# Performance work log

Hardware: AMD Instinct MI355X
Metric: run time of the kernel (lower is better)

Reference implementation:

```python
import jax, jax.numpy as jnp
import numpy as np

HID = 1024
HEADS = 16
HEAD_DIM = HID // HEADS
FFN = 4096
EPS = 1e-5


def setup_inputs() -> dict:
    key = jax.random.key(0)
    ks = jax.random.split(key, 12)
    s = lambda k, shape, fan_in: jax.random.normal(k, shape, jnp.float32) * (fan_in ** -0.5)
    return {
        "hidden_states": jax.random.normal(ks[0], (2, 2048, HID), jnp.float32),
        "Wq": s(ks[1], (HID, HID), HID),
        "Wk": s(ks[2], (HID, HID), HID),
        "Wv": s(ks[3], (HID, HID), HID),
        "Wo": s(ks[4], (HID, HID), HID),
        "W1": s(ks[5], (HID, FFN), HID),
        "b1": jnp.zeros((FFN,), jnp.float32),
        "W2": s(ks[6], (FFN, HID), FFN),
        "b2": jnp.zeros((HID,), jnp.float32),
        "ln1_scale": jnp.ones((HID,), jnp.float32),
        "ln1_shift": jnp.zeros((HID,), jnp.float32),
        "ln2_scale": jnp.ones((HID,), jnp.float32),
        "ln2_shift": jnp.zeros((HID,), jnp.float32),
    }


def _layer_norm(x, scale, shift):
    mean = jnp.mean(x, axis=-1, keepdims=True)
    var = jnp.var(x, axis=-1, keepdims=True)  # biased, matches unbiased=False
    return (x - mean) * jax.lax.rsqrt(var + EPS) * scale + shift


def _forward(hidden_states, Wq, Wk, Wv, Wo, W1, b1, W2, b2,
             ln1_scale, ln1_shift, ln2_scale, ln2_shift):
    bsz, seq_len, _ = hidden_states.shape
    residual = hidden_states
    x = _layer_norm(hidden_states, ln1_scale, ln1_shift)

    # q/k/v projections -> [b, h, s, d]
    def proj(W):
        return (x @ W).reshape(bsz, seq_len, HEADS, HEAD_DIM).transpose(0, 2, 1, 3)
    q, k, v = proj(Wq), proj(Wk), proj(Wv)

    scores = jnp.einsum("bhqd,bhkd->bhqk", q, k)
    causal = jnp.triu(jnp.ones((seq_len, seq_len), bool), k=1)
    scores = jnp.where(causal, -jnp.inf, scores) / (HEAD_DIM ** 0.5)
    attn = jax.nn.softmax(scores, axis=-1)  # dropout is identity in eval
    out = jnp.einsum("bhqk,bhkd->bhqd", attn, v)
    out = out.transpose(0, 2, 1, 3).reshape(bsz, seq_len, HID)
    hidden_states = residual + out @ Wo

    residual = hidden_states
    y = _layer_norm(hidden_states, ln2_scale, ln2_shift)
    y = jax.nn.gelu(y @ W1 + b1, approximate=False) @ W2 + b2  # torch nn.GELU default = exact erf
    return residual + y


def reference(hidden_states, Wq, Wk, Wv, Wo, W1, b1, W2, b2,
              ln1_scale, ln1_shift, ln2_scale, ln2_shift):
    return _forward(hidden_states, Wq, Wk, Wv, Wo, W1, b1, W2, b2,
                    ln1_scale, ln1_shift, ln2_scale, ln2_shift)
```

## Files before the change

### kernel.cpp

```cpp
#include <hip/hip_runtime.h>
#include <math.h>

using bf16x8 = __attribute__((ext_vector_type(8))) short;
using f32x4  = __attribute__((ext_vector_type(4))) float;

struct __align__(8) us4 { unsigned short x, y, z, w; };

__device__ __forceinline__ unsigned short f2b(float f) {
  union { float f; unsigned u; } v; v.f = f;
  unsigned r = v.u + 0x7FFFu + ((v.u >> 16) & 1u);
  return (unsigned short)(r >> 16);
}

#define GLDS(g, l) __builtin_amdgcn_global_load_lds(                        \
    (const __attribute__((address_space(1))) void*)(g),                    \
    (__attribute__((address_space(3))) void*)(l), 16, 0, 0)

__global__ void __launch_bounds__(256) transpose_w(
    const float* __restrict__ src, unsigned short* __restrict__ dst,
    int K, int N) {
  __shared__ float tile[32][33];
  const int n0 = blockIdx.x * 32, k0 = blockIdx.y * 32;
  const int tx = threadIdx.x & 31, ty = threadIdx.x >> 5;
#pragma unroll
  for (int i = 0; i < 32; i += 8)
    tile[ty + i][tx] = src[(size_t)(k0 + ty + i) * N + n0 + tx];
  __syncthreads();
#pragma unroll
  for (int i = 0; i < 32; i += 8)
    dst[(size_t)(n0 + ty + i) * K + k0 + tx] = f2b(tile[tx][ty + i]);
}

__global__ void __launch_bounds__(256) ln_kernel(
    const float* __restrict__ in, const float* __restrict__ scale,
    const float* __restrict__ shift, unsigned short* __restrict__ out) {
  const int row = blockIdx.x, t = threadIdx.x;
  const float4 v = ((const float4*)(in + (size_t)row * 1024))[t];
  float s  = v.x + v.y + v.z + v.w;
  float s2 = v.x * v.x + v.y * v.y + v.z * v.z + v.w * v.w;
#pragma unroll
  for (int off = 32; off; off >>= 1) {
    s  += __shfl_xor(s,  off);
    s2 += __shfl_xor(s2, off);
  }
  __shared__ float red[8];
  const int w = t >> 6, lane = t & 63;
  if (!lane) { red[w] = s; red[4 + w] = s2; }
  __syncthreads();
  s  = red[0] + red[1] + red[2] + red[3];
  s2 = red[4] + red[5] + red[6] + red[7];
  const float mean = s * (1.0f / 1024.0f);
  const float var  = s2 * (1.0f / 1024.0f) - mean * mean;
  const float rstd = rsqrtf(var + 1e-5f);
  const float4 sc = ((const float4*)scale)[t];
  const float4 sh = ((const float4*)shift)[t];
  us4 o;
  o.x = f2b((v.x - mean) * rstd * sc.x + sh.x);
  o.y = f2b((v.y - mean) * rstd * sc.y + sh.y);
  o.z = f2b((v.z - mean) * rstd * sc.z + sh.z);
  o.w = f2b((v.w - mean) * rstd * sc.w + sh.w);
  ((us4*)(out + (size_t)row * 1024))[t] = o;
}

template <int MODE, int BM>
__global__ void __launch_bounds__(256) gemm_bt(
    const unsigned short* __restrict__ A, const unsigned short* __restrict__ B,
    int K, int N,
    float* __restrict__ outf, unsigned short* __restrict__ outb,
    const float* __restrict__ bias, const float* __restrict__ resid,
    unsigned short* __restrict__ vt) {
  constexpr int WN = (BM == 128) ? 2 : 4;
  constexpr int NJ = 128 / (16 * WN);
  __shared__ unsigned short lA[BM * 64];
  __shared__ unsigned short lB[128 * 64];
  const int t = threadIdx.x, lane = t & 63;
  const int w = t >> 6, wm = w / WN, wn = w % WN;
  const int r16 = lane & 15, g = lane >> 4;
  const int m0 = blockIdx.x * BM, n0 = blockIdx.y * 128;

  f32x4 acc[4][NJ] = {};
  const int nkt = K >> 6;
  for (int kt = 0; kt < nkt; ++kt) {
    __syncthreads();
#pragma unroll
    for (int p = 0; p < BM / 32; ++p) {
      const int ci = t + p * 256;
      const int m = ci >> 3, cs = ci & 7;
      const int kb = cs ^ (m & 7);
      GLDS(A + (size_t)(m0 + m) * K + kt * 64 + kb * 8, &lA[ci * 8]);
    }
#pragma unroll
    for (int p = 0; p < 4; ++p) {
      const int ci = t + p * 256;
      const int m = ci >> 3, cs = ci & 7;
      const int kb = cs ^ (m & 7);
      GLDS(B + (size_t)(n0 + m) * K + kt * 64 + kb * 8, &lB[ci * 8]);
    }
    __syncthreads();
#pragma unroll
    for (int ks = 0; ks < 2; ++ks) {
      bf16x8 af[4], bfr[NJ];
#pragma unroll
      for (int i = 0; i < 4; ++i) {
        const int m = wm * 64 + i * 16 + r16;
        const int kb = ks * 4 + g;
        af[i] = *(const bf16x8*)&lA[((m << 3) + (kb ^ (m & 7))) << 3];
      }
#pragma unroll
      for (int j = 0; j < NJ; ++j) {
        const int n = wn * (16 * NJ) + j * 16 + r16;
        const int kb = ks * 4 + g;
        bfr[j] = *(const bf16x8*)&lB[((n << 3) + (kb ^ (n & 7))) << 3];
      }
#pragma unroll
      for (int i = 0; i < 4; ++i)
#pragma unroll
        for (int j = 0; j < NJ; ++j)
          acc[i][j] = __builtin_amdgcn_mfma_f32_16x16x32_bf16(
              af[i], bfr[j], acc[i][j], 0, 0, 0);
    }
  }

#pragma unroll
  for (int i = 0; i < 4; ++i) {
    const int row0 = m0 + wm * 64 + i * 16 + g * 4;
#pragma unroll
    for (int j = 0; j < NJ; ++j) {
      const int colb = n0 + wn * (16 * NJ) + j * 16;
      const int col = colb + r16;
      if constexpr (MODE == 0) {
        if (colb < 2048) {
#pragma unroll
          for (int r = 0; r < 4; ++r)
            outb[(size_t)(row0 + r) * 2048 + col] = f2b(acc[i][j][r]);
        } else {
          const int b = row0 >> 11, s0 = row0 & 2047;
          us4 pk;
          pk.x = f2b(acc[i][j][0]); pk.y = f2b(acc[i][j][1]);
          pk.z = f2b(acc[i][j][2]); pk.w = f2b(acc[i][j][3]);
          *(us4*)&vt[((size_t)b * 1024 + (col - 2048)) * 2048 + s0] = pk;
        }
      } else if constexpr (MODE == 1) {
#pragma unroll
        for (int r = 0; r < 4; ++r) {
          const size_t idx = (size_t)(row0 + r) * N + col;
          outf[idx] = acc[i][j][r] + resid[idx];
        }
      } else if constexpr (MODE == 2) {
#pragma unroll
        for (int r = 0; r < 4; ++r) {
          const float x = acc[i][j][r] + bias[col];
          const float ge = 0.5f * x * (1.0f + erff(x * 0.70710678118654752f));
          outb[(size_t)(row0 + r) * N + col] = f2b(ge);
        }
      } else {
#pragma unroll
        for (int r = 0; r < 4; ++r) {
          const size_t idx = (size_t)(row0 + r) * N + col;
          outf[idx] = acc[i][j][r] + bias[col] + resid[idx];
        }
      }
    }
  }
}

__global__ void __launch_bounds__(256) attn_kernel(
    const unsigned short* __restrict__ qk, const unsigned short* __restrict__ vt,
    unsigned short* __restrict__ obuf) {
  const int j = blockIdx.x, h = blockIdx.y, bb = blockIdx.z;
  const int t = threadIdx.x, lane = t & 63, w = t >> 6;
  const int r16 = lane & 15, g = lane >> 4;
  __shared__ unsigned short lK[2][64 * 64];
  __shared__ unsigned short lV[2][64 * 64];
  __shared__ unsigned short lP[4][16 * 72];

  const int qtA = j, qtB = 31 - j;
  const int ktmax = qtB;
  const int qrowA = qtA * 64 + w * 16 + r16;
  const int qrowB = qtB * 64 + w * 16 + r16;
  const float CE = 0.18033688011112042f;

  bf16x8 qfA[2], qfB[2];
  {
    const unsigned short* qa =
        qk + (size_t)(bb * 2048 + qrowA) * 2048 + h * 64;
    qfA[0] = *(const bf16x8*)(qa + g * 8);
    qfA[1] = *(const bf16x8*)(qa + 32 + g * 8);
    const unsigned short* qb =
        qk + (size_t)(bb * 2048 + qrowB) * 2048 + h * 64;
    qfB[0] = *(const bf16x8*)(qb + g * 8);
    qfB[1] = *(const bf16x8*)(qb + 32 + g * 8);
  }

  f32x4 accA[4] = {}, accB[4] = {};
  float mA = -3.0e38f, lA_ = 0.0f, mB = -3.0e38f, lB_ = 0.0f;

  auto stage = [&](int buf, int kt) {
    const int k0 = kt * 64;
#pragma unroll
    for (int p = 0; p < 2; ++p) {
      const int ci = t + p * 256;
      const int r = ci >> 3, cs = ci & 7;
      const int cb = cs ^ (r & 7);
      GLDS(qk + (size_t)(bb * 2048 + k0 + r) * 2048 + 1024 + h * 64 + cb * 8,
           &lK[buf][ci * 8]);
      GLDS(vt + ((size_t)bb * 1024 + h * 64 + r) * 2048 + k0 + cb * 8,
           &lV[buf][ci * 8]);
    }
  };

  auto flash_step = [&](const bf16x8* qf, f32x4* accO, float& mrun,
                        float& lrun, int qrow, bool diag, int k0, int cur) {
    f32x4 s[4] = {};
#pragma unroll
    for (int ks = 0; ks < 2; ++ks)
#pragma unroll
      for (int mt = 0; mt < 4; ++mt) {
        const int r = mt * 16 + r16, db = ks * 4 + g;
        const bf16x8 kf =
            *(const bf16x8*)&lK[cur][((r << 3) + (db ^ (r & 7))) << 3];
        s[mt] = __builtin_amdgcn_mfma_f32_16x16x32_bf16(kf, qf[ks], s[mt],
                                                        0, 0, 0);
      }
    if (diag) {
#pragma unroll
      for (int mt = 0; mt < 4; ++mt)
#pragma unroll
        for (int r = 0; r < 4; ++r)
          if (k0 + mt * 16 + g * 4 + r > qrow) s[mt][r] = -3.0e38f;
    }
    float tmax = -3.0e38f;
#pragma unroll
    for (int mt = 0; mt < 4; ++mt)
#pragma unroll
      for (int r = 0; r < 4; ++r) tmax = fmaxf(tmax, s[mt][r]);
    tmax = fmaxf(tmax, __shfl_xor(tmax, 16));
    tmax = fmaxf(tmax, __shfl_xor(tmax, 32));
    const float mnew = fmaxf(mrun, tmax);
    const float fac = __builtin_amdgcn_exp2f((mrun - mnew) * CE);
    float pv[4][4];
    float tsum = 0.0f;
#pragma unroll
    for (int mt = 0; mt < 4; ++mt)
#pragma unroll
      for (int r = 0; r < 4; ++r) {
        pv[mt][r] = __builtin_amdgcn_exp2f((s[mt][r] - mnew) * CE);
        tsum += pv[mt][r];
      }
    tsum += __shfl_xor(tsum, 16);
    tsum += __shfl_xor(tsum, 32);
    lrun = lrun * fac + tsum;
    mrun = mnew;
#pragma unroll
    for (int mt = 0; mt < 4; ++mt) {
      us4 pk;
      pk.x = f2b(pv[mt][0]); pk.y = f2b(pv[mt][1]);
      pk.z = f2b(pv[mt][2]); pk.w = f2b(pv[mt][3]);
      *(us4*)&lP[w][r16 * 72 + mt * 16 + g * 4] = pk;
    }
    float fr[4];
#pragma unroll
    for (int r = 0; r < 4; ++r) fr[r] = __shfl(fac, g * 4 + r);
#pragma unroll
    for (int nb = 0; nb < 4; ++nb)
#pragma unroll
      for (int r = 0; r < 4; ++r) accO[nb][r] *= fr[r];
#pragma unroll
    for (int ks = 0; ks < 2; ++ks) {
      const bf16x8 pa = *(const bf16x8*)&lP[w][r16 * 72 + ks * 32 + g * 8];
#pragma unroll
      for (int nb = 0; nb < 4; ++nb) {
        const int d = nb * 16 + r16, kb = ks * 4 + g;
        const bf16x8 vf =
            *(const bf16x8*)&lV[cur][((d << 3) + (kb ^ (d & 7))) << 3];
        accO[nb] = __builtin_amdgcn_mfma_f32_16x16x32_bf16(pa, vf, accO[nb],
                                                           0, 0, 0);
      }
    }
  };

  stage(0, 0);
  __syncthreads();
  int cur = 0;
  for (int kt = 0; kt <= ktmax; ++kt) {
    if (kt < ktmax) stage(cur ^ 1, kt + 1);
    flash_step(qfB, accB, mB, lB_, qrowB, kt == qtB, kt * 64, cur);
    if (kt <= qtA)
      flash_step(qfA, accA, mA, lA_, qrowA, kt == qtA, kt * 64, cur);
    __syncthreads();
    cur ^= 1;
  }

  auto epilogue = [&](const f32x4* accO, float lrun, int q0) {
    const float li = 1.0f / lrun;
    float lr_[4];
#pragma unroll
    for (int r = 0; r < 4; ++r) lr_[r] = __shfl(li, g * 4 + r);
#pragma unroll
    for (int nb = 0; nb < 4; ++nb)
#pragma unroll
      for (int r = 0; r < 4; ++r) {
        const int row = bb * 2048 + q0 + w * 16 + g * 4 + r;
        const int col = h * 64 + nb * 16 + r16;
        obuf[(size_t)row * 1024 + col] = f2b(accO[nb][r] * lr_[r]);
      }
  };
  epilogue(accA, lA_, qtA * 64);
  epilogue(accB, lB_, qtB * 64);
}

extern "C" void kernel_launch(void* const* d_in, const int* in_sizes, int n_in,
                              void* d_out, int out_size, void* d_ws,
                              size_t ws_size, hipStream_t stream) {
  const float* hs   = (const float*)d_in[0];
  const float* Wq   = (const float*)d_in[1];
  const float* Wk   = (const float*)d_in[2];
  const float* Wv   = (const float*)d_in[3];
  const float* Wo   = (const float*)d_in[4];
  const float* W1   = (const float*)d_in[5];
  const float* b1   = (const float*)d_in[6];
  const float* W2   = (const float*)d_in[7];
  const float* b2   = (const float*)d_in[8];
  const float* ln1s = (const float*)d_in[9];
  const float* ln1b = (const float*)d_in[10];
  const float* ln2s = (const float*)d_in[11];
  const float* ln2b = (const float*)d_in[12];
  float* out = (float*)d_out;

  char* ws = (char*)d_ws;
  unsigned short* wqkvT = (unsigned short*)(ws + 0);
  unsigned short* woT   = (unsigned short*)(ws + 6291456);
  unsigned short* w1T   = (unsigned short*)(ws + 8388608);
  unsigned short* w2T   = (unsigned short*)(ws + 16777216);
  float*          hid   = (float*)(ws + 25165824);
  unsigned short* xb    = (unsigned short*)(ws + 41943040);
  char*           big   = ws + 50331648;
  unsigned short* qkb   = (unsigned short*)(big);
  unsigned short* vtb   = (unsigned short*)(big + 16777216);
  unsigned short* ob    = (unsigned short*)(big + 25165824);
  unsigned short* h1    = (unsigned short*)(big);

  transpose_w<<<dim3(32, 32), 256, 0, stream>>>(Wq, wqkvT, 1024, 1024);
  transpose_w<<<dim3(32, 32), 256, 0, stream>>>(Wk, wqkvT + 1024 * 1024, 1024, 1024);
  transpose_w<<<dim3(32, 32), 256, 0, stream>>>(Wv, wqkvT + 2 * 1024 * 1024, 1024, 1024);
  transpose_w<<<dim3(32, 32), 256, 0, stream>>>(Wo, woT, 1024, 1024);
  transpose_w<<<dim3(128, 32), 256, 0, stream>>>(W1, w1T, 1024, 4096);
  transpose_w<<<dim3(32, 128), 256, 0, stream>>>(W2, w2T, 4096, 1024);

  ln_kernel<<<4096, 256, 0, stream>>>(hs, ln1s, ln1b, xb);
  gemm_bt<0, 128><<<dim3(32, 24), 256, 0, stream>>>(xb, wqkvT, 1024, 3072,
                                                    nullptr, qkb, nullptr, nullptr, vtb);
  attn_kernel<<<dim3(16, 16, 2), 256, 0, stream>>>(qkb, vtb, ob);
  gemm_bt<1, 64><<<dim3(64, 8), 256, 0, stream>>>(ob, woT, 1024, 1024,
                                                  hid, nullptr, nullptr, hs, nullptr);
  ln_kernel<<<4096, 256, 0, stream>>>(hid, ln2s, ln2b, xb);
  gemm_bt<2, 128><<<dim3(32, 32), 256, 0, stream>>>(xb, w1T, 1024, 4096,
                                                    nullptr, h1, b1, nullptr, nullptr);
  gemm_bt<3, 64><<<dim3(64, 8), 256, 0, stream>>>(h1, w2T, 4096, 1024,
                                                  out, nullptr, b2, hid, nullptr);
}
```

Measured before the change: 269.3 us.

## Double-buffer GEMM LDS tiles and use tanh-approximate GELU epilogue

Splits the GEMM shared-memory tiles into two buffers so the next k-tile's global-to-LDS loads are issued before computing on the current one, removing one barrier per iteration. LDS addresses and global source pointers are precomputed outside the loop, and bias values are loaded once per column. The exact erf GELU is replaced by a tanh approximation built from hardware exp2 and reciprocal. This doubles LDS use, which may lower occupancy, and the GELU no longer exactly matches the erf reference.

```diff
diff --git a/kernel.cpp b/kernel.cpp
--- a/kernel.cpp
+++ b/kernel.cpp
@@ -71,47 +71,69 @@
     unsigned short* __restrict__ vt) {
   constexpr int WN = (BM == 128) ? 2 : 4;
   constexpr int NJ = 128 / (16 * WN);
-  __shared__ unsigned short lA[BM * 64];
-  __shared__ unsigned short lB[128 * 64];
+  constexpr int ACH = BM / 32;
+  __shared__ unsigned short lA[2][BM * 64];
+  __shared__ unsigned short lB[2][128 * 64];
   const int t = threadIdx.x, lane = t & 63;
   const int w = t >> 6, wm = w / WN, wn = w % WN;
   const int r16 = lane & 15, g = lane >> 4;
   const int m0 = blockIdx.x * BM, n0 = blockIdx.y * 128;
 
+  const unsigned short* aSrc[ACH];
+  const unsigned short* bSrc[4];
+#pragma unroll
+  for (int p = 0; p < ACH; ++p) {
+    const int ci = t + p * 256, m = ci >> 3, cs = ci & 7;
+    aSrc[p] = A + (size_t)(m0 + m) * K + (cs ^ (m & 7)) * 8;
+  }
+#pragma unroll
+  for (int p = 0; p < 4; ++p) {
+    const int ci = t + p * 256, m = ci >> 3, cs = ci & 7;
+    bSrc[p] = B + (size_t)(n0 + m) * K + (cs ^ (m & 7)) * 8;
+  }
+
+  int aOff[4][2], bOff[NJ][2];
+#pragma unroll
+  for (int i = 0; i < 4; ++i)
+#pragma unroll
+    for (int ks = 0; ks < 2; ++ks) {
+      const int m = wm * 64 + i * 16 + r16, kb = ks * 4 + g;
+      aOff[i][ks] = ((m << 3) + (kb ^ (m & 7))) << 3;
+    }
+#pragma unroll
+  for (int j = 0; j < NJ; ++j)
+#pragma unroll
+    for (int ks = 0; ks < 2; ++ks) {
+      const int n = wn * (16 * NJ) + j * 16 + r16, kb = ks * 4 + g;
+      bOff[j][ks] = ((n << 3) + (kb ^ (n & 7))) << 3;
+    }
+
+  auto stage = [&](int buf, int kt) {
+    const int off = kt * 64;
+#pragma unroll
+    for (int p = 0; p < ACH; ++p)
+      GLDS(aSrc[p] + off, &lA[buf][(t + p * 256) * 8]);
+#pragma unroll
+    for (int p = 0; p < 4; ++p)
+      GLDS(bSrc[p] + off, &lB[buf][(t + p * 256) * 8]);
+  };
+
   f32x4 acc[4][NJ] = {};
   const int nkt = K >> 6;
+  stage(0, 0);
+  __syncthreads();
   for (int kt = 0; kt < nkt; ++kt) {
-    __syncthreads();
-#pragma unroll
-    for (int p = 0; p < BM / 32; ++p) {
-      const int ci = t + p * 256;
-      const int m = ci >> 3, cs = ci & 7;
-      const int kb = cs ^ (m & 7);
-      GLDS(A + (size_t)(m0 + m) * K + kt * 64 + kb * 8, &lA[ci * 8]);
-    }
-#pragma unroll
-    for (int p = 0; p < 4; ++p) {
-      const int ci = t + p * 256;
-      const int m = ci >> 3, cs = ci & 7;
-      const int kb = cs ^ (m & 7);
-      GLDS(B + (size_t)(n0 + m) * K + kt * 64 + kb * 8, &lB[ci * 8]);
-    }
-    __syncthreads();
+    const int cur = kt & 1;
+    if (kt + 1 < nkt) stage(cur ^ 1, kt + 1);
+    const unsigned short* bA = lA[cur];
+    const unsigned short* bB = lB[cur];
 #pragma unroll
     for (int ks = 0; ks < 2; ++ks) {
       bf16x8 af[4], bfr[NJ];
 #pragma unroll
-      for (int i = 0; i < 4; ++i) {
-        const int m = wm * 64 + i * 16 + r16;
-        const int kb = ks * 4 + g;
-        af[i] = *(const bf16x8*)&lA[((m << 3) + (kb ^ (m & 7))) << 3];
-      }
-#pragma unroll
-      for (int j = 0; j < NJ; ++j) {
-        const int n = wn * (16 * NJ) + j * 16 + r16;
-        const int kb = ks * 4 + g;
-        bfr[j] = *(const bf16x8*)&lB[((n << 3) + (kb ^ (n & 7))) << 3];
-      }
+      for (int i = 0; i < 4; ++i) af[i] = *(const bf16x8*)&bA[aOff[i][ks]];
+#pragma unroll
+      for (int j = 0; j < NJ; ++j) bfr[j] = *(const bf16x8*)&bB[bOff[j][ks]];
 #pragma unroll
       for (int i = 0; i < 4; ++i)
 #pragma unroll
@@ -119,8 +141,15 @@
           acc[i][j] = __builtin_amdgcn_mfma_f32_16x16x32_bf16(
               af[i], bfr[j], acc[i][j], 0, 0, 0);
     }
-  }
-
+    __syncthreads();
+  }
+
+  float bj[NJ];
+  if constexpr (MODE == 2 || MODE == 3) {
+#pragma unroll
+    for (int j = 0; j < NJ; ++j)
+      bj[j] = bias[n0 + wn * (16 * NJ) + j * 16 + r16];
+  }
 #pragma unroll
   for (int i = 0; i < 4; ++i) {
     const int row0 = m0 + wm * 64 + i * 16 + g * 4;
@@ -149,15 +178,17 @@
       } else if constexpr (MODE == 2) {
 #pragma unroll
         for (int r = 0; r < 4; ++r) {
-          const float x = acc[i][j][r] + bias[col];
-          const float ge = 0.5f * x * (1.0f + erff(x * 0.70710678118654752f));
-          outb[(size_t)(row0 + r) * N + col] = f2b(ge);
+          const float x = acc[i][j][r] + bj[j];
+          const float u = x * (0.7978845608028654f + 0.03567740814f * x * x);
+          const float e = __builtin_amdgcn_exp2f(u * 2.885390081777927f);
+          const float th = 1.0f - 2.0f * __builtin_amdgcn_rcpf(e + 1.0f);
+          outb[(size_t)(row0 + r) * N + col] = f2b(0.5f * x * (1.0f + th));
         }
       } else {
 #pragma unroll
         for (int r = 0; r < 4; ++r) {
           const size_t idx = (size_t)(row0 + r) * N + col;
-          outf[idx] = acc[i][j][r] + bias[col] + resid[idx];
+          outf[idx] = acc[i][j][r] + bj[j] + resid[idx];
         }
       }
     }
```

After: 245.1 us. 1.1x faster.
